# Performance work log

Hardware: AMD Instinct MI355X
Metric: run time of the kernel (lower is better)

Reference implementation:

```python
import jax, jax.numpy as jnp
import numpy as np

B, S, D_MODEL, D_K, D_V = 8, 2048, 1024, 1024, 1024


def setup_inputs() -> dict:
    key = jax.random.key(0)
    k1, k2, k3, k4 = jax.random.split(key, 4)
    x = jax.random.normal(k1, (B, S, D_MODEL), dtype=jnp.float32)
    # Store projection weights as [d_model, d_out] so projection is x @ W
    # (equivalent to torch Linear(d_model, d_out, bias=False) with W^T).
    scale = 1.0 / np.sqrt(D_MODEL)
    Wq = jax.random.normal(k2, (D_MODEL, D_K), dtype=jnp.float32) * scale
    Wk = jax.random.normal(k3, (D_MODEL, D_K), dtype=jnp.float32) * scale
    Wv = jax.random.normal(k4, (D_MODEL, D_V), dtype=jnp.float32) * scale
    return {"x": x, "Wq": Wq, "Wk": Wk, "Wv": Wv}


def reference(x, Wq, Wk, Wv):
    # Single-head causal self-attention, faithful to the original:
    # NOTE: the original scales by sqrt(x.shape[-1]) == sqrt(d_model),
    # not sqrt(d_k of the projection).
    Q = jnp.einsum('bsd,dk->bsk', x, Wq)
    K = jnp.einsum('bsd,dk->bsk', x, Wk)
    V = jnp.einsum('bsd,dv->bsv', x, Wv)
    inv_scale = 1.0 / jnp.sqrt(jnp.asarray(x.shape[-1], x.dtype))
    A = jnp.einsum('bqk,bsk->bqs', Q, K) * inv_scale  # [B, S, S]
    S_len = A.shape[-1]
    causal = jnp.tril(jnp.ones((S_len, S_len), dtype=bool))  # [S, S]
    A = jnp.where(causal, A, -jnp.inf)
    P = jax.nn.softmax(A, axis=-1)
    return jnp.einsum('bqs,bsv->bqv', P, V)
```

## Files before the change

### kernel.cpp

```cpp
#include <hip/hip_runtime.h>
#include <hip/hip_bf16.h>
#include <stdint.h>


typedef __bf16 bf16_t;
typedef __bf16 bf16x4 __attribute__((ext_vector_type(4)));
typedef __bf16 bf16x8 __attribute__((ext_vector_type(8)));
typedef float  floatx4 __attribute__((ext_vector_type(4)));

#define NB 8
#define SS 2048
#define DD 1024
#define INV_SCALE 0.03125f

__device__ __forceinline__ void async_ld16(const void* g, void* l) {
  __builtin_amdgcn_global_load_lds(
      (const __attribute__((address_space(1))) void*)g,
      (__attribute__((address_space(3))) void*)l, 16, 0, 0);
}

__device__ __forceinline__ void mm_core(const bf16_t* __restrict__ Ab,
                                        const bf16_t* __restrict__ Bb,
                                        int lda, int ldb, int kTiles,
                                        bf16_t* sA, bf16_t* sB,
                                        floatx4 acc[4][4]) {
  const int t    = threadIdx.x;
  const int lane = t & 63;
  const int wm   = (t >> 6) >> 1;
  const int wn   = (t >> 6) & 1;
  const int sr   = t >> 2;
  const int sc   = (t & 3) * 8;
  const int fm   = lane & 15;
  const int fk   = (lane >> 4) * 8;

  const bf16_t* ga0 = Ab + (size_t)sr * lda + sc;
  const bf16_t* ga1 = Ab + (size_t)(sr + 64) * lda + sc;
  const bf16_t* gb0 = Bb + (size_t)sr * ldb + sc;
  const bf16_t* gb1 = Bb + (size_t)(sr + 64) * ldb + sc;
  bf16_t* la0 = sA + t * 8;
  bf16_t* la1 = sA + (t + 256) * 8;
  bf16_t* lb0 = sB + t * 8;
  bf16_t* lb1 = sB + (t + 256) * 8;

  const bf16_t* pa = sA + (wm * 64 + fm) * 32 + fk;
  const bf16_t* pb = sB + (wn * 64 + fm) * 32 + fk;

  for (int kt = 0; kt < kTiles; ++kt) {
    const int ko = kt * 32;
    async_ld16(ga0 + ko, la0);
    async_ld16(ga1 + ko, la1);
    async_ld16(gb0 + ko, lb0);
    async_ld16(gb1 + ko, lb1);
    __syncthreads();
    bf16x8 af[4], bfr[4];
#pragma unroll
    for (int i = 0; i < 4; ++i) af[i]  = *(const bf16x8*)(pa + i * 512);
#pragma unroll
    for (int j = 0; j < 4; ++j) bfr[j] = *(const bf16x8*)(pb + j * 512);
#pragma unroll
    for (int i = 0; i < 4; ++i)
#pragma unroll
      for (int j = 0; j < 4; ++j)
        acc[i][j] = __builtin_amdgcn_mfma_f32_16x16x32_bf16(af[i], bfr[j], acc[i][j], 0, 0, 0);
    __syncthreads();
  }
}

__device__ __forceinline__ void zero_acc(floatx4 acc[4][4]) {
#pragma unroll
  for (int i = 0; i < 4; ++i)
#pragma unroll
    for (int j = 0; j < 4; ++j)
      acc[i][j] = floatx4{0.f, 0.f, 0.f, 0.f};
}


__global__ __launch_bounds__(256) void cvt_x(const float* __restrict__ in,
                                             bf16_t* __restrict__ out) {
  size_t i = (size_t)blockIdx.x * 256 + threadIdx.x;
  float4 v = ((const float4*)in)[i];
  bf16x4 o = {(bf16_t)v.x, (bf16_t)v.y, (bf16_t)v.z, (bf16_t)v.w};
  ((bf16x4*)out)[i] = o;
}

__global__ __launch_bounds__(256) void cvt_w_t(const float* __restrict__ Wq,
                                               const float* __restrict__ Wk,
                                               const float* __restrict__ Wv,
                                               bf16_t* __restrict__ Wt) {
  const int z = blockIdx.z;
  const float* W = (z == 0) ? Wq : (z == 1 ? Wk : Wv);
  bf16_t* O = Wt + (size_t)z * DD * DD;
  __shared__ float tile[32][33];
  const int t  = threadIdx.x;
  const int ty = t >> 3;
  const int tx = t & 7;
  const int k0 = blockIdx.x * 32, n0 = blockIdx.y * 32;
  float4 v = *(const float4*)(W + (size_t)(k0 + ty) * DD + n0 + tx * 4);
  tile[ty][tx * 4 + 0] = v.x;
  tile[ty][tx * 4 + 1] = v.y;
  tile[ty][tx * 4 + 2] = v.z;
  tile[ty][tx * 4 + 3] = v.w;
  __syncthreads();
  bf16x4 o = {(bf16_t)tile[tx * 4 + 0][ty], (bf16_t)tile[tx * 4 + 1][ty],
              (bf16_t)tile[tx * 4 + 2][ty], (bf16_t)tile[tx * 4 + 3][ty]};
  *(bf16x4*)(O + (size_t)(n0 + ty) * DD + k0 + tx * 4) = o;
}


__global__ __launch_bounds__(256) void gemm_bf16(
    const bf16_t* __restrict__ A, const bf16_t* __restrict__ B,
    bf16_t* __restrict__ C, int lda, int ldb, int ldc, int kTiles,
    unsigned long long aStride, unsigned long long bStride, unsigned long long cStride) {
  __shared__ __attribute__((aligned(16))) bf16_t sA[128 * 32];
  __shared__ __attribute__((aligned(16))) bf16_t sB[128 * 32];
  const int mt = blockIdx.x, nt = blockIdx.y, bz = blockIdx.z;
  const bf16_t* Ab = A + (size_t)bz * aStride + (size_t)mt * 128 * lda;
  const bf16_t* Bb = B + (size_t)bz * bStride + (size_t)nt * 128 * ldb;
  bf16_t* Cb = C + (size_t)bz * cStride + (size_t)mt * 128 * ldc + nt * 128;
  floatx4 acc[4][4];
  zero_acc(acc);
  mm_core(Ab, Bb, lda, ldb, kTiles, sA, sB, acc);
  const int lane = threadIdx.x & 63;
  const int wm = (threadIdx.x >> 6) >> 1, wn = (threadIdx.x >> 6) & 1;
  const int r0 = wm * 64 + (lane >> 4) * 4;
  const int c0 = wn * 64 + (lane & 15);
#pragma unroll
  for (int i = 0; i < 4; ++i)
#pragma unroll
    for (int j = 0; j < 4; ++j)
#pragma unroll
      for (int r = 0; r < 4; ++r)
        Cb[(size_t)(r0 + i * 16 + r) * ldc + c0 + j * 16] = (bf16_t)acc[i][j][r];
}


__global__ __launch_bounds__(256) void qk_p(
    const bf16_t* __restrict__ Q, const bf16_t* __restrict__ K,
    bf16_t* __restrict__ P, float* __restrict__ lpart) {
  const int tt = blockIdx.x;
  int qi = (int)((sqrtf(8.0f * tt + 1.0f) - 1.0f) * 0.5f);
  while ((qi + 1) * (qi + 2) / 2 <= tt) ++qi;
  while (qi * (qi + 1) / 2 > tt) --qi;
  const int ki = tt - qi * (qi + 1) / 2;
  const int b = blockIdx.z;

  __shared__ __attribute__((aligned(16))) bf16_t sA[128 * 32];
  __shared__ __attribute__((aligned(16))) bf16_t sB[128 * 32];
  __shared__ float reds[2][128];
  const bf16_t* Ab = Q + ((size_t)b * SS + qi * 128) * (size_t)(2 * DD);
  const bf16_t* Bb = K + ((size_t)b * SS + ki * 128) * (size_t)(2 * DD);
  floatx4 acc[4][4];
  zero_acc(acc);
  mm_core(Ab, Bb, 2 * DD, 2 * DD, DD / 32, sA, sB, acc);

  const int lane = threadIdx.x & 63;
  const int wm = (threadIdx.x >> 6) >> 1, wn = (threadIdx.x >> 6) & 1;
  const bool diag = (ki == qi);
  bf16_t* Pb = P + (size_t)b * SS * SS;

#pragma unroll
  for (int i = 0; i < 4; ++i)
#pragma unroll
    for (int r = 0; r < 4; ++r) {
      const int row = wm * 64 + i * 16 + (lane >> 4) * 4 + r;
      float partial = 0.f;
#pragma unroll
      for (int j = 0; j < 4; ++j) {
        const int col = wn * 64 + j * 16 + (lane & 15);
        const float s = acc[i][j][r] * INV_SCALE;
        const float p = (diag && col > row) ? 0.f : __expf(s);
        partial += p;
        Pb[(size_t)(qi * 128 + row) * SS + ki * 128 + col] = (bf16_t)p;
      }
#pragma unroll
      for (int d = 1; d < 16; d <<= 1) partial += __shfl_xor(partial, d);
      if ((lane & 15) == 0) reds[wn][row] = partial;
    }
  __syncthreads();
  const int t = threadIdx.x;
  if (t < 128) {
    size_t row = (size_t)b * SS + qi * 128 + t;
    lpart[row * 16 + ki] = reds[0][t] + reds[1][t];
  }
}

__global__ __launch_bounds__(256) void lsum(
    const float* __restrict__ lpart, float* __restrict__ rl) {
  const int idx = blockIdx.x * 256 + threadIdx.x;
  const int q = idx & (SS - 1);
  const int nch = (q >> 7) + 1;
  const float* lp = lpart + (size_t)idx * 16;
  float L = 0.f;
  for (int c = 0; c < nch; ++c) L += lp[c];
  rl[idx] = 1.0f / L;
}


__global__ __launch_bounds__(256) void pv_gemm(
    const bf16_t* __restrict__ P, const bf16_t* __restrict__ Vt,
    const float* __restrict__ rl, float* __restrict__ Out) {
  const int i  = blockIdx.x;
  const int c  = i & 255;
  const int k  = i >> 8;
  const int q0 = c & 15;
  const int h  = c >> 4;
  const int qi = (k & 1) ? (15 - q0) : q0;
  const int nj = h & 7;
  const int b  = (h >> 3) | (k << 1);

  __shared__ __attribute__((aligned(16))) bf16_t sA[128 * 32];
  __shared__ __attribute__((aligned(16))) bf16_t sB[128 * 32];
  const bf16_t* Ab = P + (size_t)b * SS * SS + (size_t)qi * 128 * SS;
  const bf16_t* Bb = Vt + (size_t)b * DD * SS + (size_t)nj * 128 * SS;
  float* Cb = Out + (size_t)b * SS * DD + (size_t)qi * 128 * DD + nj * 128;
  floatx4 acc[4][4];
  zero_acc(acc);
  mm_core(Ab, Bb, SS, SS, (qi + 1) * 4, sA, sB, acc);
  const int lane = threadIdx.x & 63;
  const int wm = (threadIdx.x >> 6) >> 1, wn = (threadIdx.x >> 6) & 1;
  const int r0 = wm * 64 + (lane >> 4) * 4;
  const int c0 = wn * 64 + (lane & 15);
  const float* rlb = rl + (size_t)b * SS + qi * 128;
#pragma unroll
  for (int i2 = 0; i2 < 4; ++i2)
#pragma unroll
    for (int r = 0; r < 4; ++r) {
      const float scale = rlb[r0 + i2 * 16 + r];
#pragma unroll
      for (int j = 0; j < 4; ++j)
        Cb[(size_t)(r0 + i2 * 16 + r) * DD + c0 + j * 16] = acc[i2][j][r] * scale;
    }
}


extern "C" void kernel_launch(void* const* d_in, const int* in_sizes, int n_in,
                              void* d_out, int out_size, void* d_ws, size_t ws_size,
                              hipStream_t stream) {
  const float* x  = (const float*)d_in[0];
  const float* Wq = (const float*)d_in[1];
  const float* Wk = (const float*)d_in[2];
  const float* Wv = (const float*)d_in[3];
  float* out = (float*)d_out;

  char* ws = (char*)d_ws;
  bf16_t* xb   = (bf16_t*)(ws);
  bf16_t* Wt   = (bf16_t*)(ws + 33554432ull);
  bf16_t* QKb  = (bf16_t*)(ws + 39845888ull);
  bf16_t* VtB  = (bf16_t*)(ws + 106954752ull);
  bf16_t* Pb   = (bf16_t*)(ws + 140509184ull);
  float*  lpart= (float*)(ws + 207618048ull);
  float*  rl   = (float*)(ws + 208666624ull);
  (void)in_sizes; (void)n_in; (void)out_size; (void)ws_size;

  cvt_x<<<16384, 256, 0, stream>>>(x, xb);
  cvt_w_t<<<dim3(32, 32, 3), 256, 0, stream>>>(Wq, Wk, Wv, Wt);
  gemm_bf16<<<dim3(128, 16, 1), 256, 0, stream>>>(xb, Wt, QKb, DD, DD, 2 * DD, DD / 32, 0, 0, 0);
  gemm_bf16<<<dim3(8, 16, NB), 256, 0, stream>>>(Wt + 2097152, xb, VtB, DD, DD, SS, DD / 32,
                                                 0ull, (unsigned long long)SS * DD,
                                                 (unsigned long long)DD * SS);
  qk_p<<<dim3(136, 1, NB), 256, 0, stream>>>(QKb, QKb + DD, Pb, lpart);
  lsum<<<64, 256, 0, stream>>>(lpart, rl);
  pv_gemm<<<1024, 256, 0, stream>>>(Pb, VtB, rl, out);
}
```

Baseline: 428.3 us.

## Swap MFMA operands for row-contiguous accumulators, vectorize epilogue stores, merge prep kernels

The MFMA operand order is swapped so each lane's four accumulator values lie along the N (column) dimension. This lets the GEMM, QK-softmax and PV epilogues write bf16x4 or float4 vectors instead of scalar strided stores. The row-sum reduction in qk_p changes to match, shuffling across lane groups instead of within 16 lanes. The x-conversion and weight-transpose kernels are merged into a single launch to save one kernel launch.

```diff
diff --git a/kernel.cpp b/kernel.cpp
--- a/kernel.cpp
+++ b/kernel.cpp
@@ -61,7 +61,7 @@
     for (int i = 0; i < 4; ++i)
 #pragma unroll
       for (int j = 0; j < 4; ++j)
-        acc[i][j] = __builtin_amdgcn_mfma_f32_16x16x32_bf16(af[i], bfr[j], acc[i][j], 0, 0, 0);
+        acc[i][j] = __builtin_amdgcn_mfma_f32_16x16x32_bf16(bfr[j], af[i], acc[i][j], 0, 0, 0);
     __syncthreads();
   }
 }
@@ -75,35 +75,39 @@
 }
 
 
-__global__ __launch_bounds__(256) void cvt_x(const float* __restrict__ in,
-                                             bf16_t* __restrict__ out) {
-  size_t i = (size_t)blockIdx.x * 256 + threadIdx.x;
-  float4 v = ((const float4*)in)[i];
-  bf16x4 o = {(bf16_t)v.x, (bf16_t)v.y, (bf16_t)v.z, (bf16_t)v.w};
-  ((bf16x4*)out)[i] = o;
-}
-
-__global__ __launch_bounds__(256) void cvt_w_t(const float* __restrict__ Wq,
-                                               const float* __restrict__ Wk,
-                                               const float* __restrict__ Wv,
-                                               bf16_t* __restrict__ Wt) {
-  const int z = blockIdx.z;
-  const float* W = (z == 0) ? Wq : (z == 1 ? Wk : Wv);
-  bf16_t* O = Wt + (size_t)z * DD * DD;
+__global__ __launch_bounds__(256) void prep(const float* __restrict__ x,
+                                            const float* __restrict__ Wq,
+                                            const float* __restrict__ Wk,
+                                            const float* __restrict__ Wv,
+                                            bf16_t* __restrict__ xb,
+                                            bf16_t* __restrict__ Wt) {
   __shared__ float tile[32][33];
-  const int t  = threadIdx.x;
-  const int ty = t >> 3;
-  const int tx = t & 7;
-  const int k0 = blockIdx.x * 32, n0 = blockIdx.y * 32;
-  float4 v = *(const float4*)(W + (size_t)(k0 + ty) * DD + n0 + tx * 4);
-  tile[ty][tx * 4 + 0] = v.x;
-  tile[ty][tx * 4 + 1] = v.y;
-  tile[ty][tx * 4 + 2] = v.z;
-  tile[ty][tx * 4 + 3] = v.w;
-  __syncthreads();
-  bf16x4 o = {(bf16_t)tile[tx * 4 + 0][ty], (bf16_t)tile[tx * 4 + 1][ty],
-              (bf16_t)tile[tx * 4 + 2][ty], (bf16_t)tile[tx * 4 + 3][ty]};
-  *(bf16x4*)(O + (size_t)(n0 + ty) * DD + k0 + tx * 4) = o;
+  const int bid = blockIdx.x;
+  const int t = threadIdx.x;
+  if (bid < 16384) {
+    size_t i = (size_t)bid * 256 + t;
+    float4 v = ((const float4*)x)[i];
+    bf16x4 o = {(bf16_t)v.x, (bf16_t)v.y, (bf16_t)v.z, (bf16_t)v.w};
+    ((bf16x4*)xb)[i] = o;
+  } else {
+    const int wb = bid - 16384;
+    const int z = wb >> 10;
+    const int rem = wb & 1023;
+    const float* W = (z == 0) ? Wq : (z == 1 ? Wk : Wv);
+    bf16_t* O = Wt + (size_t)z * DD * DD;
+    const int ty = t >> 3;
+    const int tx = t & 7;
+    const int k0 = (rem >> 5) * 32, n0 = (rem & 31) * 32;
+    float4 v = *(const float4*)(W + (size_t)(k0 + ty) * DD + n0 + tx * 4);
+    tile[ty][tx * 4 + 0] = v.x;
+    tile[ty][tx * 4 + 1] = v.y;
+    tile[ty][tx * 4 + 2] = v.z;
+    tile[ty][tx * 4 + 3] = v.w;
+    __syncthreads();
+    bf16x4 o = {(bf16_t)tile[tx * 4 + 0][ty], (bf16_t)tile[tx * 4 + 1][ty],
+                (bf16_t)tile[tx * 4 + 2][ty], (bf16_t)tile[tx * 4 + 3][ty]};
+    *(bf16x4*)(O + (size_t)(n0 + ty) * DD + k0 + tx * 4) = o;
+  }
 }
 
 
@@ -122,15 +126,16 @@
   mm_core(Ab, Bb, lda, ldb, kTiles, sA, sB, acc);
   const int lane = threadIdx.x & 63;
   const int wm = (threadIdx.x >> 6) >> 1, wn = (threadIdx.x >> 6) & 1;
-  const int r0 = wm * 64 + (lane >> 4) * 4;
-  const int c0 = wn * 64 + (lane & 15);
+  const int m0 = wm * 64 + (lane & 15);
+  const int n0 = wn * 64 + (lane >> 4) * 4;
 #pragma unroll
   for (int i = 0; i < 4; ++i)
 #pragma unroll
-    for (int j = 0; j < 4; ++j)
-#pragma unroll
-      for (int r = 0; r < 4; ++r)
-        Cb[(size_t)(r0 + i * 16 + r) * ldc + c0 + j * 16] = (bf16_t)acc[i][j][r];
+    for (int j = 0; j < 4; ++j) {
+      floatx4 a = acc[i][j];
+      bf16x4 o = {(bf16_t)a[0], (bf16_t)a[1], (bf16_t)a[2], (bf16_t)a[3]};
+      *(bf16x4*)(Cb + (size_t)(m0 + i * 16) * ldc + n0 + j * 16) = o;
+    }
 }
 
 
@@ -157,25 +162,30 @@
   const int wm = (threadIdx.x >> 6) >> 1, wn = (threadIdx.x >> 6) & 1;
   const bool diag = (ki == qi);
   bf16_t* Pb = P + (size_t)b * SS * SS;
-
-#pragma unroll
-  for (int i = 0; i < 4; ++i)
-#pragma unroll
-    for (int r = 0; r < 4; ++r) {
-      const int row = wm * 64 + i * 16 + (lane >> 4) * 4 + r;
-      float partial = 0.f;
-#pragma unroll
-      for (int j = 0; j < 4; ++j) {
-        const int col = wn * 64 + j * 16 + (lane & 15);
+  const int qloc0 = wm * 64 + (lane & 15);
+  const int kvb0  = wn * 64 + (lane >> 4) * 4;
+
+#pragma unroll
+  for (int i = 0; i < 4; ++i) {
+    const int qrow = qloc0 + i * 16;
+    float partial = 0.f;
+#pragma unroll
+    for (int j = 0; j < 4; ++j) {
+      const int kvb = kvb0 + j * 16;
+      floatx4 p;
+#pragma unroll
+      for (int r = 0; r < 4; ++r) {
         const float s = acc[i][j][r] * INV_SCALE;
-        const float p = (diag && col > row) ? 0.f : __expf(s);
-        partial += p;
-        Pb[(size_t)(qi * 128 + row) * SS + ki * 128 + col] = (bf16_t)p;
+        p[r] = (diag && (kvb + r) > qrow) ? 0.f : __expf(s);
+        partial += p[r];
       }
-#pragma unroll
-      for (int d = 1; d < 16; d <<= 1) partial += __shfl_xor(partial, d);
-      if ((lane & 15) == 0) reds[wn][row] = partial;
+      bf16x4 o = {(bf16_t)p[0], (bf16_t)p[1], (bf16_t)p[2], (bf16_t)p[3]};
+      *(bf16x4*)(Pb + (size_t)(qi * 128 + qrow) * SS + ki * 128 + kvb) = o;
     }
+    partial += __shfl_xor(partial, 16);
+    partial += __shfl_xor(partial, 32);
+    if ((lane >> 4) == 0) reds[wn][qrow] = partial;
+  }
   __syncthreads();
   const int t = threadIdx.x;
   if (t < 128) {
@@ -218,18 +228,20 @@
   mm_core(Ab, Bb, SS, SS, (qi + 1) * 4, sA, sB, acc);
   const int lane = threadIdx.x & 63;
   const int wm = (threadIdx.x >> 6) >> 1, wn = (threadIdx.x >> 6) & 1;
-  const int r0 = wm * 64 + (lane >> 4) * 4;
-  const int c0 = wn * 64 + (lane & 15);
+  const int m0 = wm * 64 + (lane & 15);
+  const int n0 = wn * 64 + (lane >> 4) * 4;
   const float* rlb = rl + (size_t)b * SS + qi * 128;
 #pragma unroll
-  for (int i2 = 0; i2 < 4; ++i2)
-#pragma unroll
-    for (int r = 0; r < 4; ++r) {
-      const float scale = rlb[r0 + i2 * 16 + r];
-#pragma unroll
-      for (int j = 0; j < 4; ++j)
-        Cb[(size_t)(r0 + i2 * 16 + r) * DD + c0 + j * 16] = acc[i2][j][r] * scale;
+  for (int i2 = 0; i2 < 4; ++i2) {
+    const float scale = rlb[m0 + i2 * 16];
+    float* crow = Cb + (size_t)(m0 + i2 * 16) * DD + n0;
+#pragma unroll
+    for (int j = 0; j < 4; ++j) {
+      floatx4 o = acc[i2][j];
+      o[0] *= scale; o[1] *= scale; o[2] *= scale; o[3] *= scale;
+      *(floatx4*)(crow + j * 16) = o;
     }
+  }
 }
 
 
@@ -252,8 +264,7 @@
   float*  rl   = (float*)(ws + 208666624ull);
   (void)in_sizes; (void)n_in; (void)out_size; (void)ws_size;
 
-  cvt_x<<<16384, 256, 0, stream>>>(x, xb);
-  cvt_w_t<<<dim3(32, 32, 3), 256, 0, stream>>>(Wq, Wk, Wv, Wt);
+  prep<<<16384 + 3072, 256, 0, stream>>>(x, Wq, Wk, Wv, xb, Wt);
   gemm_bf16<<<dim3(128, 16, 1), 256, 0, stream>>>(xb, Wt, QKb, DD, DD, 2 * DD, DD / 32, 0, 0, 0);
   gemm_bf16<<<dim3(8, 16, NB), 256, 0, stream>>>(Wt + 2097152, xb, VtB, DD, DD, SS, DD / 32,
                                                  0ull, (unsigned long long)SS * DD,
```

Measured after the change: 442.6 us. 1.03x slower.
